# Optimization experiments

Hardware: AMD Instinct MI355X
Metric: run time of the kernel (lower is better)

Reference implementation:

```python
import jax, jax.numpy as jnp
import numpy as np

N_NODES = 100000
N_EDGES = 1600000
D_IN = 64
D_OUT = 64


def setup_inputs() -> dict:
    key = jax.random.key(0)
    k1, k2, k3, k4 = jax.random.split(key, 4)
    x = jax.random.normal(k1, (N_NODES, D_IN), dtype=jnp.float32)
    edge_index = jax.random.randint(k2, (2, N_EDGES), 0, N_NODES, dtype=jnp.int64)
    # MLP params (torch Linear stores [out,in]; here stored [in,out] for x @ W)
    s1 = (6.0 / (D_IN + D_OUT)) ** 0.5  # xavier_uniform bound
    s2 = (6.0 / (D_OUT + D_OUT)) ** 0.5
    W1 = jax.random.uniform(k3, (D_IN, D_OUT), dtype=jnp.float32, minval=-s1, maxval=s1)
    b1 = jnp.zeros((D_OUT,), dtype=jnp.float32)
    W2 = jax.random.uniform(k4, (D_OUT, D_OUT), dtype=jnp.float32, minval=-s2, maxval=s2)
    b2 = jnp.zeros((D_OUT,), dtype=jnp.float32)
    return {"x": x, "edge_index": edge_index, "W1": W1, "b1": b1, "W2": W2, "b2": b2}


def reference(x, edge_index, W1, b1, W2, b2):
    # Eval mode: F.dropout is identity when training=False.
    src, dst = edge_index[0], edge_index[1]
    # GIN aggregation: sum of neighbor features scattered to destination nodes
    agg = jax.ops.segment_sum(x[src], dst, num_segments=N_NODES)  # [N, D_IN]
    h = x + agg  # (1 + eps) * x + agg, eps = 0 (GINConv default)
    h = jax.nn.relu(h @ W1 + b1)
    return h @ W2 + b2
```

## Files before the change

### kernel.cpp

```cpp
#include <hip/hip_runtime.h>

#define N_NODES 100000
#define N_EDGES 1600000

#define SPAN 256
#define NB 391
#define NBLK_A 256
#define EPB (N_EDGES / NBLK_A)

#define SCAN_CHUNK 2048
#define SCAN_BLOCKS ((N_NODES + SCAN_CHUNK - 1) / SCAN_CHUNK)

typedef __attribute__((ext_vector_type(8))) short bf16x8;
typedef __attribute__((ext_vector_type(4))) float f32x4;

static __device__ __forceinline__ unsigned short f2bf(float f) {
    unsigned u = __float_as_uint(f);
    unsigned r = (u + 0x7FFF + ((u >> 16) & 1)) >> 16;
    return (unsigned short)r;
}


__global__ __launch_bounds__(256) void count_buckets(const int* __restrict__ ei,
                                                     int* __restrict__ M) {
    __shared__ int hist[NB];
    int tid = threadIdx.x;
    for (int i = tid; i < NB; i += 256) hist[i] = 0;
    __syncthreads();
    int e0 = blockIdx.x * EPB;
    for (int e = e0 + tid; e < e0 + EPB; e += 256)
        atomicAdd(&hist[ei[N_EDGES + e] >> 8], 1);
    __syncthreads();
    for (int i = tid; i < NB; i += 256) M[blockIdx.x * NB + i] = hist[i];
}

__global__ void col_scan(int* __restrict__ M, int* __restrict__ bcount) {
    int b = blockIdx.x * blockDim.x + threadIdx.x;
    if (b >= NB) return;
    int s = 0;
    for (int k = 0; k < NBLK_A; ++k) {
        int idx = k * NB + b;
        int t = M[idx];
        M[idx] = s;
        s += t;
    }
    bcount[b] = s;
}

__global__ __launch_bounds__(512) void bucket_base(const int* __restrict__ bcount,
                                                   int* __restrict__ bbase) {
    __shared__ int s[512];
    int tid = threadIdx.x;
    int v = (tid < NB) ? bcount[tid] : 0;
    s[tid] = v;
    __syncthreads();
    for (int off = 1; off < 512; off <<= 1) {
        int t = (tid >= off) ? s[tid - off] : 0;
        __syncthreads();
        s[tid] += t;
        __syncthreads();
    }
    if (tid < NB) bbase[tid] = s[tid] - v;
    if (tid == NB - 1) bbase[NB] = s[tid];
}

__global__ __launch_bounds__(256) void bin_edges(const int* __restrict__ ei,
                                                 const int* __restrict__ M,
                                                 const int* __restrict__ bbase,
                                                 int* __restrict__ binned) {
    __shared__ int sbase[NB];
    __shared__ int cur[NB];
    int tid = threadIdx.x;
    for (int i = tid; i < NB; i += 256) {
        sbase[i] = bbase[i] + M[blockIdx.x * NB + i];
        cur[i] = 0;
    }
    __syncthreads();
    int e0 = blockIdx.x * EPB;
    for (int e = e0 + tid; e < e0 + EPB; e += 256) {
        int d = ei[N_EDGES + e];
        int s = ei[e];
        int b = d >> 8;
        int r = atomicAdd(&cur[b], 1);
        binned[sbase[b] + r] = (s << 8) | (d & 255);
    }
}

__global__ __launch_bounds__(256) void bucket_sort(const int* __restrict__ binned,
                                                   const int* __restrict__ bbase,
                                                   int* __restrict__ csr,
                                                   int* __restrict__ offs) {
    __shared__ int lh[256];
    __shared__ int ls[256];
    __shared__ int lc[256];
    int tid = threadIdx.x;
    int b = blockIdx.x;
    int base = bbase[b];
    int cnt = bbase[b + 1] - base;

    lh[tid] = 0;
    __syncthreads();
    for (int i = tid; i < cnt; i += 256)
        atomicAdd(&lh[binned[base + i] & 255], 1);
    __syncthreads();

    int own = lh[tid];
    ls[tid] = own;
    __syncthreads();
    for (int off = 1; off < 256; off <<= 1) {
        int t = (tid >= off) ? ls[tid - off] : 0;
        __syncthreads();
        ls[tid] += t;
        __syncthreads();
    }

    int node = b * SPAN + tid;
    if (node < N_NODES) offs[node] = base + ls[tid];

    int ex = ls[tid] - own;
    __syncthreads();
    ls[tid] = ex;
    lc[tid] = 0;
    __syncthreads();
    for (int i = tid; i < cnt; i += 256) {
        int en = binned[base + i];
        int ld = en & 255;
        int r = atomicAdd(&lc[ld], 1);
        csr[base + ls[ld] + r] = en >> 8;
    }
}

__global__ __launch_bounds__(512) void gather_mfma(
    const float4* __restrict__ x4, const int* __restrict__ offs,
    const int* __restrict__ csr, float* __restrict__ out,
    const float* __restrict__ W1, const float* __restrict__ b1,
    const float* __restrict__ W2, const float* __restrict__ b2) {

    __shared__ unsigned short shA[16][72];
    __shared__ unsigned short sh1[16][72];
    __shared__ unsigned short W1t[64][72];
    __shared__ unsigned short W2t[64][72];

    int tid = threadIdx.x;
    int w = tid >> 6;
    int lane = tid & 63;

    {
        int k = tid >> 3;
        int j0 = (tid & 7) * 8;
        float4 wa = *(const float4*)&W1[k * 64 + j0];
        float4 wb = *(const float4*)&W1[k * 64 + j0 + 4];
        W1t[j0 + 0][k] = f2bf(wa.x); W1t[j0 + 1][k] = f2bf(wa.y);
        W1t[j0 + 2][k] = f2bf(wa.z); W1t[j0 + 3][k] = f2bf(wa.w);
        W1t[j0 + 4][k] = f2bf(wb.x); W1t[j0 + 5][k] = f2bf(wb.y);
        W1t[j0 + 6][k] = f2bf(wb.z); W1t[j0 + 7][k] = f2bf(wb.w);
        wa = *(const float4*)&W2[k * 64 + j0];
        wb = *(const float4*)&W2[k * 64 + j0 + 4];
        W2t[j0 + 0][k] = f2bf(wa.x); W2t[j0 + 1][k] = f2bf(wa.y);
        W2t[j0 + 2][k] = f2bf(wa.z); W2t[j0 + 3][k] = f2bf(wa.w);
        W2t[j0 + 4][k] = f2bf(wb.x); W2t[j0 + 5][k] = f2bf(wb.y);
        W2t[j0 + 6][k] = f2bf(wb.z); W2t[j0 + 7][k] = f2bf(wb.w);
    }

    int s = lane >> 4;
    int c = lane & 15;
    int nA = blockIdx.x * 16 + 2 * w;
    int nB = nA + 1;
    int stA = (nA == 0) ? 0 : offs[nA - 1];
    int enA = offs[nA];
    int stB = offs[nB - 1];
    int enB = offs[nB];

    float4 accA = make_float4(0.f, 0.f, 0.f, 0.f);
    float4 accB = accA;
    if (s == 0) {
        accA = x4[(size_t)nA * 16 + c];
        accB = x4[(size_t)nB * 16 + c];
    }

    for (int bA = stA, bB = stB; bA < enA || bB < enB; bA += 16, bB += 16) {
        int pA = bA + s, pB = bB + s;
        int a0 = (pA      < enA) ? csr[pA]      : -1;
        int a1 = (pA + 4  < enA) ? csr[pA + 4]  : -1;
        int a2 = (pA + 8  < enA) ? csr[pA + 8]  : -1;
        int a3 = (pA + 12 < enA) ? csr[pA + 12] : -1;
        int b0 = (pB      < enB) ? csr[pB]      : -1;
        int b1i = (pB + 4 < enB) ? csr[pB + 4]  : -1;
        int b2i = (pB + 8 < enB) ? csr[pB + 8]  : -1;
        int b3i = (pB + 12 < enB) ? csr[pB + 12] : -1;
        float4 vA0 = x4[(size_t)max(a0, 0) * 16 + c];
        float4 vA1 = x4[(size_t)max(a1, 0) * 16 + c];
        float4 vA2 = x4[(size_t)max(a2, 0) * 16 + c];
        float4 vA3 = x4[(size_t)max(a3, 0) * 16 + c];
        float4 vB0 = x4[(size_t)max(b0, 0) * 16 + c];
        float4 vB1 = x4[(size_t)max(b1i, 0) * 16 + c];
        float4 vB2 = x4[(size_t)max(b2i, 0) * 16 + c];
        float4 vB3 = x4[(size_t)max(b3i, 0) * 16 + c];
        if (a0 >= 0) { accA.x += vA0.x; accA.y += vA0.y; accA.z += vA0.z; accA.w += vA0.w; }
        if (a1 >= 0) { accA.x += vA1.x; accA.y += vA1.y; accA.z += vA1.z; accA.w += vA1.w; }
        if (a2 >= 0) { accA.x += vA2.x; accA.y += vA2.y; accA.z += vA2.z; accA.w += vA2.w; }
        if (a3 >= 0) { accA.x += vA3.x; accA.y += vA3.y; accA.z += vA3.z; accA.w += vA3.w; }
        if (b0 >= 0) { accB.x += vB0.x; accB.y += vB0.y; accB.z += vB0.z; accB.w += vB0.w; }
        if (b1i >= 0) { accB.x += vB1.x; accB.y += vB1.y; accB.z += vB1.z; accB.w += vB1.w; }
        if (b2i >= 0) { accB.x += vB2.x; accB.y += vB2.y; accB.z += vB2.z; accB.w += vB2.w; }
        if (b3i >= 0) { accB.x += vB3.x; accB.y += vB3.y; accB.z += vB3.z; accB.w += vB3.w; }
    }

    accA.x += __shfl_xor(accA.x, 16); accA.y += __shfl_xor(accA.y, 16);
    accA.z += __shfl_xor(accA.z, 16); accA.w += __shfl_xor(accA.w, 16);
    accA.x += __shfl_xor(accA.x, 32); accA.y += __shfl_xor(accA.y, 32);
    accA.z += __shfl_xor(accA.z, 32); accA.w += __shfl_xor(accA.w, 32);
    accB.x += __shfl_xor(accB.x, 16); accB.y += __shfl_xor(accB.y, 16);
    accB.z += __shfl_xor(accB.z, 16); accB.w += __shfl_xor(accB.w, 16);
    accB.x += __shfl_xor(accB.x, 32); accB.y += __shfl_xor(accB.y, 32);
    accB.z += __shfl_xor(accB.z, 32); accB.w += __shfl_xor(accB.w, 32);

    if (s == 0) {
        ushort4 ra, rb;
        ra.x = f2bf(accA.x); ra.y = f2bf(accA.y);
        ra.z = f2bf(accA.z); ra.w = f2bf(accA.w);
        rb.x = f2bf(accB.x); rb.y = f2bf(accB.y);
        rb.z = f2bf(accB.z); rb.w = f2bf(accB.w);
        *(ushort4*)&shA[2 * w][c * 4] = ra;
        *(ushort4*)&shA[2 * w + 1][c * 4] = rb;
    }
    __syncthreads();

    if (w < 4) {
        int row = lane & 15;
        int kg = lane >> 4;
        int jj = w * 16 + (lane & 15);
        bf16x8 a0 = *(bf16x8*)&shA[row][kg * 8];
        bf16x8 a1 = *(bf16x8*)&shA[row][32 + kg * 8];
        bf16x8 w0 = *(bf16x8*)&W1t[jj][kg * 8];
        bf16x8 w1 = *(bf16x8*)&W1t[jj][32 + kg * 8];
        f32x4 d = {0.f, 0.f, 0.f, 0.f};
        d = __builtin_amdgcn_mfma_f32_16x16x32_bf16(a0, w0, d, 0, 0, 0);
        d = __builtin_amdgcn_mfma_f32_16x16x32_bf16(a1, w1, d, 0, 0, 0);
        float bias = b1[jj];
#pragma unroll
        for (int i = 0; i < 4; ++i) {
            float v = fmaxf(d[i] + bias, 0.f);
            sh1[kg * 4 + i][jj] = f2bf(v);
        }
    }
    __syncthreads();

    if (w < 4) {
        int row = lane & 15;
        int kg = lane >> 4;
        int jj = w * 16 + (lane & 15);
        bf16x8 a0 = *(bf16x8*)&sh1[row][kg * 8];
        bf16x8 a1 = *(bf16x8*)&sh1[row][32 + kg * 8];
        bf16x8 w0 = *(bf16x8*)&W2t[jj][kg * 8];
        bf16x8 w1 = *(bf16x8*)&W2t[jj][32 + kg * 8];
        f32x4 d = {0.f, 0.f, 0.f, 0.f};
        d = __builtin_amdgcn_mfma_f32_16x16x32_bf16(a0, w0, d, 0, 0, 0);
        d = __builtin_amdgcn_mfma_f32_16x16x32_bf16(a1, w1, d, 0, 0, 0);
        float bias = b2[jj];
        int nbase = blockIdx.x * 16 + kg * 4;
#pragma unroll
        for (int i = 0; i < 4; ++i)
            out[(size_t)(nbase + i) * 64 + jj] = d[i] + bias;
    }
}

__global__ __launch_bounds__(512) void gather_mlp(
    const float4* __restrict__ x4, const int* __restrict__ offs,
    const int* __restrict__ csr, float* __restrict__ out,
    const float* __restrict__ W1, const float* __restrict__ b1,
    const float* __restrict__ W2, const float* __restrict__ b2) {
    __shared__ float sW1[64][64];
    __shared__ float sW2[64][64];
    __shared__ float sb1[64];
    __shared__ float sb2[64];
    __shared__ float sh[8][64];
    __shared__ float sh1[8][64];

    int tid = threadIdx.x;
    for (int i = tid; i < 4096; i += 512) {
        sW1[i >> 6][i & 63] = W1[i];
        sW2[i >> 6][i & 63] = W2[i];
    }
    if (tid < 64) {
        sb1[tid] = b1[tid];
        sb2[tid] = b2[tid];
    }

    int local = tid >> 6;
    int lane = tid & 63;
    int s = lane >> 4;
    int c = lane & 15;
    int node = blockIdx.x * 8 + local;

    int start = (node == 0) ? 0 : offs[node - 1];
    int end = offs[node];

    float4 acc = make_float4(0.f, 0.f, 0.f, 0.f);
    float4 self = x4[(size_t)node * 16 + c];
    if (s == 0) acc = self;

    for (int b = start; b < end; b += 16) {
        int p = b + s;
        int i0 = (p < end) ? csr[p] : -1;
        int i1 = (p + 4 < end) ? csr[p + 4] : -1;
        int i2 = (p + 8 < end) ? csr[p + 8] : -1;
        int i3 = (p + 12 < end) ? csr[p + 12] : -1;
        float4 v0 = x4[(size_t)max(i0, 0) * 16 + c];
        float4 v1 = x4[(size_t)max(i1, 0) * 16 + c];
        float4 v2 = x4[(size_t)max(i2, 0) * 16 + c];
        float4 v3 = x4[(size_t)max(i3, 0) * 16 + c];
        if (i0 >= 0) { acc.x += v0.x; acc.y += v0.y; acc.z += v0.z; acc.w += v0.w; }
        if (i1 >= 0) { acc.x += v1.x; acc.y += v1.y; acc.z += v1.z; acc.w += v1.w; }
        if (i2 >= 0) { acc.x += v2.x; acc.y += v2.y; acc.z += v2.z; acc.w += v2.w; }
        if (i3 >= 0) { acc.x += v3.x; acc.y += v3.y; acc.z += v3.z; acc.w += v3.w; }
    }

    acc.x += __shfl_xor(acc.x, 16); acc.y += __shfl_xor(acc.y, 16);
    acc.z += __shfl_xor(acc.z, 16); acc.w += __shfl_xor(acc.w, 16);
    acc.x += __shfl_xor(acc.x, 32); acc.y += __shfl_xor(acc.y, 32);
    acc.z += __shfl_xor(acc.z, 32); acc.w += __shfl_xor(acc.w, 32);

    __syncthreads();
    if (s == 0) *(float4*)&sh[local][c * 4] = acc;
    __syncthreads();

    int j = lane;
    float a1 = sb1[j];
#pragma unroll
    for (int k = 0; k < 64; ++k) a1 = fmaf(sh[local][k], sW1[k][j], a1);
    a1 = fmaxf(a1, 0.0f);
    sh1[local][j] = a1;
    __syncthreads();

    float a2 = sb2[j];
#pragma unroll
    for (int k = 0; k < 64; ++k) a2 = fmaf(sh1[local][k], sW2[k][j], a2);
    out[(size_t)node * 64 + j] = a2;
}

__global__ void zero_ints(int* __restrict__ p, int n) {
    int i = blockIdx.x * blockDim.x + threadIdx.x;
    if (i < n) p[i] = 0;
}

__global__ void count_deg(const int* __restrict__ ei, int* __restrict__ deg) {
    int e = blockIdx.x * blockDim.x + threadIdx.x;
    if (e < N_EDGES) atomicAdd(&deg[ei[N_EDGES + e]], 1);
}

__global__ __launch_bounds__(256) void scan_a(const int* __restrict__ deg,
                                              int* __restrict__ offs,
                                              int* __restrict__ bsum) {
    __shared__ int lds[256];
    int tid = threadIdx.x;
    int base = blockIdx.x * SCAN_CHUNK + tid * 8;
    int v[8], ex[8];
    int run = 0;
#pragma unroll
    for (int k = 0; k < 8; ++k) {
        v[k] = (base + k < N_NODES) ? deg[base + k] : 0;
        ex[k] = run;
        run += v[k];
    }
    lds[tid] = run;
    __syncthreads();
    for (int off = 1; off < 256; off <<= 1) {
        int t = (tid >= off) ? lds[tid - off] : 0;
        __syncthreads();
        lds[tid] += t;
        __syncthreads();
    }
    int prefix = lds[tid] - run;
#pragma unroll
    for (int k = 0; k < 8; ++k)
        if (base + k < N_NODES) offs[base + k] = prefix + ex[k];
    if (tid == 0) bsum[blockIdx.x] = lds[255];
}

__global__ void scan_c(int* __restrict__ offs, const int* __restrict__ bsum) {
    int i = blockIdx.x * blockDim.x + threadIdx.x;
    if (i >= N_NODES) return;
    int chunk = i / SCAN_CHUNK;
    int add = 0;
    for (int t = 0; t < chunk; ++t) add += bsum[t];
    offs[i] += add;
}

__global__ void fill_csr(const int* __restrict__ ei, int* __restrict__ offs,
                         int* __restrict__ csr) {
    int e = blockIdx.x * blockDim.x + threadIdx.x;
    if (e >= N_EDGES) return;
    int src = ei[e];
    int dst = ei[N_EDGES + e];
    int pos = atomicAdd(&offs[dst], 1);
    csr[pos] = src;
}

__global__ void init_h(const float4* __restrict__ x, float4* __restrict__ h,
                       int n4) {
    int i = blockIdx.x * blockDim.x + threadIdx.x;
    if (i < n4) h[i] = x[i];
}

__global__ void scatter_add(const float4* __restrict__ x4,
                            const int* __restrict__ ei,
                            float* __restrict__ h) {
    long long i = (long long)blockIdx.x * blockDim.x + threadIdx.x;
    if (i >= (long long)N_EDGES * 16) return;
    int e = (int)(i >> 4);
    int lane = (int)(i & 15);
    int src = ei[e];
    int dst = ei[N_EDGES + e];
    float4 v = x4[(long long)src * 16 + lane];
    float* p = h + (long long)dst * 64 + lane * 4;
    unsafeAtomicAdd(p + 0, v.x);
    unsafeAtomicAdd(p + 1, v.y);
    unsafeAtomicAdd(p + 2, v.z);
    unsafeAtomicAdd(p + 3, v.w);
}

__global__ __launch_bounds__(256) void mlp(float* __restrict__ h,
                                           const float* __restrict__ W1,
                                           const float* __restrict__ b1,
                                           const float* __restrict__ W2,
                                           const float* __restrict__ b2) {
    __shared__ float sW1[64][64];
    __shared__ float sW2[64][64];
    __shared__ float sb1[64];
    __shared__ float sb2[64];
    __shared__ float sh[4][64];
    __shared__ float sh1[4][64];
    int tid = threadIdx.x;
    for (int i = tid; i < 4096; i += 256) {
        sW1[i >> 6][i & 63] = W1[i];
        sW2[i >> 6][i & 63] = W2[i];
    }
    if (tid < 64) { sb1[tid] = b1[tid]; sb2[tid] = b2[tid]; }
    __syncthreads();
    int local = tid >> 6, j = tid & 63;
    int node = blockIdx.x * 4 + local;
    sh[local][j] = h[(long long)node * 64 + j];
    __syncthreads();
    float acc = sb1[j];
#pragma unroll
    for (int k = 0; k < 64; ++k) acc = fmaf(sh[local][k], sW1[k][j], acc);
    acc = fmaxf(acc, 0.0f);
    sh1[local][j] = acc;
    __syncthreads();
    float acc2 = sb2[j];
#pragma unroll
    for (int k = 0; k < 64; ++k) acc2 = fmaf(sh1[local][k], sW2[k][j], acc2);
    h[(long long)node * 64 + j] = acc2;
}

extern "C" void kernel_launch(void* const* d_in, const int* in_sizes, int n_in,
                              void* d_out, int out_size, void* d_ws, size_t ws_size,
                              hipStream_t stream) {
    const float* x = (const float*)d_in[0];
    const int* ei = (const int*)d_in[1];
    const float* W1 = (const float*)d_in[2];
    const float* b1 = (const float*)d_in[3];
    const float* W2 = (const float*)d_in[4];
    const float* b2 = (const float*)d_in[5];
    float* out = (float*)d_out;

    size_t need_csr = (size_t)(N_NODES + NBLK_A * NB + NB + (NB + 1) +
                               2 * N_EDGES) * sizeof(int);
    size_t need_mid = (size_t)(2 * N_NODES + SCAN_BLOCKS + N_EDGES) * sizeof(int);

    if (ws_size >= need_csr) {
        int* offs = (int*)d_ws;
        int* M = offs + N_NODES;
        int* bcount = M + NBLK_A * NB;
        int* bbase = bcount + NB;
        int* binned = bbase + (NB + 1);
        int* csr = binned + N_EDGES;

        count_buckets<<<NBLK_A, 256, 0, stream>>>(ei, M);
        col_scan<<<(NB + 255) / 256, 256, 0, stream>>>(M, bcount);
        bucket_base<<<1, 512, 0, stream>>>(bcount, bbase);
        bin_edges<<<NBLK_A, 256, 0, stream>>>(ei, M, bbase, binned);
        bucket_sort<<<NB, 256, 0, stream>>>(binned, bbase, csr, offs);
        gather_mfma<<<N_NODES / 16, 512, 0, stream>>>((const float4*)x, offs,
                                                      csr, out, W1, b1, W2, b2);
    } else if (ws_size >= need_mid) {
        int* deg = (int*)d_ws;
        int* offs = deg + N_NODES;
        int* bsum = offs + N_NODES;
        int* csr = bsum + SCAN_BLOCKS;

        zero_ints<<<(N_NODES + 255) / 256, 256, 0, stream>>>(deg, N_NODES);
        count_deg<<<(N_EDGES + 255) / 256, 256, 0, stream>>>(ei, deg);
        scan_a<<<SCAN_BLOCKS, 256, 0, stream>>>(deg, offs, bsum);
        scan_c<<<(N_NODES + 255) / 256, 256, 0, stream>>>(offs, bsum);
        fill_csr<<<(N_EDGES + 255) / 256, 256, 0, stream>>>(ei, offs, csr);
        gather_mlp<<<N_NODES / 8, 512, 0, stream>>>((const float4*)x, offs,
                                                    csr, out, W1, b1, W2, b2);
    } else {
        int n4 = N_NODES * 64 / 4;
        init_h<<<(n4 + 255) / 256, 256, 0, stream>>>((const float4*)x,
                                                     (float4*)out, n4);
        long long nwork = (long long)N_EDGES * 16;
        scatter_add<<<(int)((nwork + 255) / 256), 256, 0, stream>>>(
            (const float4*)x, ei, out);
        mlp<<<N_NODES / 4, 256, 0, stream>>>(out, W1, b1, W2, b2);
    }
}
```

Before: 124.1 us.

## Widen sort kernels to 512 threads, vectorize weight staging, split MLP waves

The count, bin and bucket-sort kernels now run with 512 threads per block instead of 256, with the bucket-sort scan steps guarded to the first 256 threads. Weight transposition into LDS now uses coalesced column reads and packed 16-byte LDS stores in place of scattered 2-byte stores. The second MLP layer moves to waves 4-7, which preload their W2 fragments before the first layer finishes, so idle waves take part in the work. The changes target latency in the preprocessing and the fused gather kernel, but the extra threads add more shared-atomic contention and more idle lanes in the scan steps.

```diff
diff --git a/kernel.cpp b/kernel.cpp
--- a/kernel.cpp
+++ b/kernel.cpp
@@ -21,17 +21,17 @@
 }
 
 
-__global__ __launch_bounds__(256) void count_buckets(const int* __restrict__ ei,
+__global__ __launch_bounds__(512) void count_buckets(const int* __restrict__ ei,
                                                      int* __restrict__ M) {
     __shared__ int hist[NB];
     int tid = threadIdx.x;
-    for (int i = tid; i < NB; i += 256) hist[i] = 0;
+    for (int i = tid; i < NB; i += 512) hist[i] = 0;
     __syncthreads();
     int e0 = blockIdx.x * EPB;
-    for (int e = e0 + tid; e < e0 + EPB; e += 256)
+    for (int e = e0 + tid; e < e0 + EPB; e += 512)
         atomicAdd(&hist[ei[N_EDGES + e] >> 8], 1);
     __syncthreads();
-    for (int i = tid; i < NB; i += 256) M[blockIdx.x * NB + i] = hist[i];
+    for (int i = tid; i < NB; i += 512) M[blockIdx.x * NB + i] = hist[i];
 }
 
 __global__ void col_scan(int* __restrict__ M, int* __restrict__ bcount) {
@@ -64,20 +64,20 @@
     if (tid == NB - 1) bbase[NB] = s[tid];
 }
 
-__global__ __launch_bounds__(256) void bin_edges(const int* __restrict__ ei,
+__global__ __launch_bounds__(512) void bin_edges(const int* __restrict__ ei,
                                                  const int* __restrict__ M,
                                                  const int* __restrict__ bbase,
                                                  int* __restrict__ binned) {
     __shared__ int sbase[NB];
     __shared__ int cur[NB];
     int tid = threadIdx.x;
-    for (int i = tid; i < NB; i += 256) {
+    for (int i = tid; i < NB; i += 512) {
         sbase[i] = bbase[i] + M[blockIdx.x * NB + i];
         cur[i] = 0;
     }
     __syncthreads();
     int e0 = blockIdx.x * EPB;
-    for (int e = e0 + tid; e < e0 + EPB; e += 256) {
+    for (int e = e0 + tid; e < e0 + EPB; e += 512) {
         int d = ei[N_EDGES + e];
         int s = ei[e];
         int b = d >> 8;
@@ -86,7 +86,7 @@
     }
 }
 
-__global__ __launch_bounds__(256) void bucket_sort(const int* __restrict__ binned,
+__global__ __launch_bounds__(512) void bucket_sort(const int* __restrict__ binned,
                                                    const int* __restrict__ bbase,
                                                    int* __restrict__ csr,
                                                    int* __restrict__ offs) {
@@ -98,31 +98,38 @@
     int base = bbase[b];
     int cnt = bbase[b + 1] - base;
 
-    lh[tid] = 0;
-    __syncthreads();
-    for (int i = tid; i < cnt; i += 256)
+    if (tid < 256) lh[tid] = 0;
+    __syncthreads();
+    for (int i = tid; i < cnt; i += 512)
         atomicAdd(&lh[binned[base + i] & 255], 1);
     __syncthreads();
 
-    int own = lh[tid];
-    ls[tid] = own;
+    int own = 0;
+    if (tid < 256) {
+        own = lh[tid];
+        ls[tid] = own;
+    }
     __syncthreads();
     for (int off = 1; off < 256; off <<= 1) {
-        int t = (tid >= off) ? ls[tid - off] : 0;
+        int t = (tid < 256 && tid >= off) ? ls[tid - off] : 0;
         __syncthreads();
-        ls[tid] += t;
+        if (tid < 256) ls[tid] += t;
         __syncthreads();
     }
 
-    int node = b * SPAN + tid;
-    if (node < N_NODES) offs[node] = base + ls[tid];
-
-    int ex = ls[tid] - own;
-    __syncthreads();
-    ls[tid] = ex;
-    lc[tid] = 0;
-    __syncthreads();
-    for (int i = tid; i < cnt; i += 256) {
+    if (tid < 256) {
+        int node = b * SPAN + tid;
+        if (node < N_NODES) offs[node] = base + ls[tid];
+    }
+
+    int ex = (tid < 256) ? (ls[tid] - own) : 0;
+    __syncthreads();
+    if (tid < 256) {
+        ls[tid] = ex;
+        lc[tid] = 0;
+    }
+    __syncthreads();
+    for (int i = tid; i < cnt; i += 512) {
         int en = binned[base + i];
         int ld = en & 255;
         int r = atomicAdd(&lc[ld], 1);
@@ -146,20 +153,20 @@
     int lane = tid & 63;
 
     {
-        int k = tid >> 3;
-        int j0 = (tid & 7) * 8;
-        float4 wa = *(const float4*)&W1[k * 64 + j0];
-        float4 wb = *(const float4*)&W1[k * 64 + j0 + 4];
-        W1t[j0 + 0][k] = f2bf(wa.x); W1t[j0 + 1][k] = f2bf(wa.y);
-        W1t[j0 + 2][k] = f2bf(wa.z); W1t[j0 + 3][k] = f2bf(wa.w);
-        W1t[j0 + 4][k] = f2bf(wb.x); W1t[j0 + 5][k] = f2bf(wb.y);
-        W1t[j0 + 6][k] = f2bf(wb.z); W1t[j0 + 7][k] = f2bf(wb.w);
-        wa = *(const float4*)&W2[k * 64 + j0];
-        wb = *(const float4*)&W2[k * 64 + j0 + 4];
-        W2t[j0 + 0][k] = f2bf(wa.x); W2t[j0 + 1][k] = f2bf(wa.y);
-        W2t[j0 + 2][k] = f2bf(wa.z); W2t[j0 + 3][k] = f2bf(wa.w);
-        W2t[j0 + 4][k] = f2bf(wb.x); W2t[j0 + 5][k] = f2bf(wb.y);
-        W2t[j0 + 6][k] = f2bf(wb.z); W2t[j0 + 7][k] = f2bf(wb.w);
+        int j = lane;
+        int kc = w;
+        unsigned p1[4], p2[4];
+#pragma unroll
+        for (int h = 0; h < 4; ++h) {
+            float a0 = W1[(kc * 8 + 2 * h) * 64 + j];
+            float a1 = W1[(kc * 8 + 2 * h + 1) * 64 + j];
+            p1[h] = (unsigned)f2bf(a0) | ((unsigned)f2bf(a1) << 16);
+            float c0 = W2[(kc * 8 + 2 * h) * 64 + j];
+            float c1 = W2[(kc * 8 + 2 * h + 1) * 64 + j];
+            p2[h] = (unsigned)f2bf(c0) | ((unsigned)f2bf(c1) << 16);
+        }
+        *(uint4*)&W1t[j][kc * 8] = make_uint4(p1[0], p1[1], p1[2], p1[3]);
+        *(uint4*)&W2t[j][kc * 8] = make_uint4(p2[0], p2[1], p2[2], p2[3]);
     }
 
     int s = lane >> 4;
@@ -226,10 +233,18 @@
     }
     __syncthreads();
 
+    int row = lane & 15;
+    int kg = lane >> 4;
+
+    bf16x8 w20, w21;
+    if (w >= 4) {
+        int jj = (w - 4) * 16 + row;
+        w20 = *(bf16x8*)&W2t[jj][kg * 8];
+        w21 = *(bf16x8*)&W2t[jj][32 + kg * 8];
+    }
+
     if (w < 4) {
-        int row = lane & 15;
-        int kg = lane >> 4;
-        int jj = w * 16 + (lane & 15);
+        int jj = w * 16 + row;
         bf16x8 a0 = *(bf16x8*)&shA[row][kg * 8];
         bf16x8 a1 = *(bf16x8*)&shA[row][32 + kg * 8];
         bf16x8 w0 = *(bf16x8*)&W1t[jj][kg * 8];
@@ -246,17 +261,13 @@
     }
     __syncthreads();
 
-    if (w < 4) {
-        int row = lane & 15;
-        int kg = lane >> 4;
-        int jj = w * 16 + (lane & 15);
+    if (w >= 4) {
+        int jj = (w - 4) * 16 + row;
         bf16x8 a0 = *(bf16x8*)&sh1[row][kg * 8];
         bf16x8 a1 = *(bf16x8*)&sh1[row][32 + kg * 8];
-        bf16x8 w0 = *(bf16x8*)&W2t[jj][kg * 8];
-        bf16x8 w1 = *(bf16x8*)&W2t[jj][32 + kg * 8];
         f32x4 d = {0.f, 0.f, 0.f, 0.f};
-        d = __builtin_amdgcn_mfma_f32_16x16x32_bf16(a0, w0, d, 0, 0, 0);
-        d = __builtin_amdgcn_mfma_f32_16x16x32_bf16(a1, w1, d, 0, 0, 0);
+        d = __builtin_amdgcn_mfma_f32_16x16x32_bf16(a0, w20, d, 0, 0, 0);
+        d = __builtin_amdgcn_mfma_f32_16x16x32_bf16(a1, w21, d, 0, 0, 0);
         float bias = b2[jj];
         int nbase = blockIdx.x * 16 + kg * 4;
 #pragma unroll
@@ -477,11 +488,11 @@
         int* binned = bbase + (NB + 1);
         int* csr = binned + N_EDGES;
 
-        count_buckets<<<NBLK_A, 256, 0, stream>>>(ei, M);
+        count_buckets<<<NBLK_A, 512, 0, stream>>>(ei, M);
         col_scan<<<(NB + 255) / 256, 256, 0, stream>>>(M, bcount);
         bucket_base<<<1, 512, 0, stream>>>(bcount, bbase);
-        bin_edges<<<NBLK_A, 256, 0, stream>>>(ei, M, bbase, binned);
-        bucket_sort<<<NB, 256, 0, stream>>>(binned, bbase, csr, offs);
+        bin_edges<<<NBLK_A, 512, 0, stream>>>(ei, M, bbase, binned);
+        bucket_sort<<<NB, 512, 0, stream>>>(binned, bbase, csr, offs);
         gather_mfma<<<N_NODES / 16, 512, 0, stream>>>((const float4*)x, offs,
                                                       csr, out, W1, b1, W2, b2);
     } else if (ws_size >= need_mid) {
```

New measurement: 112.2 us. 9.6% less time.
